# Performance work log

Measured on AMD Instinct MI355X. Metric: run time of the kernel, lower is better.

## Reference

```python
import jax, jax.numpy as jnp
import numpy as np
import math

N = 256  # channels == model dim M
B, H, W = 8, 48, 48
EPS = 1e-5


def _kaiming(key, shape, a=math.sqrt(5)):
    # kaiming_normal_ with fan_in = shape[1] (2D weight), leaky_relu gain
    fan_in = shape[1]
    gain = math.sqrt(2.0 / (1.0 + a * a))
    std = gain / math.sqrt(fan_in)
    return std * jax.random.normal(key, shape, dtype=jnp.float32)


def setup_inputs() -> dict:
    key = jax.random.key(0)
    ks = jax.random.split(key, 6)
    x_l = jax.random.normal(ks[0], (B, N, H, W), dtype=jnp.float32)
    x_r = jax.random.normal(ks[1], (B, N, H, W), dtype=jnp.float32)
    Wq = _kaiming(ks[2], (N, N))
    Wk = _kaiming(ks[3], (N, N))
    Wv = _kaiming(ks[4], (N, N))
    Wo = _kaiming(ks[5], (N, N))
    g1 = jnp.ones((N,), jnp.float32); b1 = jnp.zeros((N,), jnp.float32)
    g2 = jnp.ones((N,), jnp.float32); b2 = jnp.zeros((N,), jnp.float32)
    return {"x_l": x_l, "x_r": x_r, "Wq": Wq, "Wk": Wk, "Wv": Wv, "Wo": Wo,
            "g1": g1, "b1": b1, "g2": g2, "b2": b2}


def _layernorm(x, g, b):
    mu = jnp.mean(x, axis=-1, keepdims=True)
    var = jnp.mean(jnp.square(x - mu), axis=-1, keepdims=True)
    return (x - mu) * jax.lax.rsqrt(var + EPS) * g + b


def reference(x_l, x_r, Wq, Wk, Wv, Wo, g1, b1, g2, b2):
    Bsz, C, Hh, Ww = x_l.shape
    S = Hh * Ww
    # [B, C, H, W] -> [B, S, C]
    xl = x_l.reshape(Bsz, C, S).transpose(0, 2, 1)
    xr = x_r.reshape(Bsz, C, S).transpose(0, 2, 1)
    xln_l = _layernorm(xl, g1, b1)
    xln_r = _layernorm(xr, g2, b2)
    Ql = xln_l @ Wq; Qr = xln_r @ Wq
    Kl = xln_l @ Wk; Kr = xln_r @ Wk
    Vl = xln_l @ Wv; Vr = xln_r @ Wv
    scale = 1.0 / math.sqrt(C)
    Al = jnp.einsum('bsc,btc->bst', Ql, Kr) * scale  # [B,S,S]
    Ar = jnp.einsum('bsc,btc->bst', Qr, Kl) * scale
    # NOTE: original uses nn.Softmax() with dim=None; for a 3-D tensor torch's
    # legacy _get_softmax_dim resolves to dim=0 (over batch). Faithfully replicated.
    Pl = jax.nn.softmax(Al, axis=0)
    Pr = jax.nn.softmax(Ar, axis=0)
    out_l = xl + (Pl @ Vl) @ Wo
    out_r = xr + (Pr @ Vr) @ Wo
    out_l = out_l.transpose(0, 2, 1).reshape(Bsz, C, Hh, Ww)
    out_r = out_r.transpose(0, 2, 1).reshape(Bsz, C, Hh, Ww)
    return out_l, out_r
```

## Files before the change

### kernel.cpp

```cpp
#include <hip/hip_runtime.h>
#include <stdint.h>

#define SDIM 2304
#define CDIM 256
#define NB   8
#define MTOT (NB * SDIM)

typedef __attribute__((ext_vector_type(8))) short short8;
typedef __attribute__((ext_vector_type(4))) float f32x4;

__device__ __forceinline__ float b2f(unsigned short h) {
  union { unsigned int u; float f; } v; v.u = ((unsigned int)h) << 16; return v.f;
}
__device__ __forceinline__ unsigned short f2b(float f) {
  union { unsigned int u; float f; } v; v.f = f;
  unsigned int u = v.u;
  u += 0x7fffu + ((u >> 16) & 1u);
  return (unsigned short)(u >> 16);
}
static inline unsigned short f2b_host(float f) {
  union { unsigned int u; float f; } v; v.f = f;
  unsigned int u = v.u;
  u += 0x7fffu + ((u >> 16) & 1u);
  return (unsigned short)(u >> 16);
}

__device__ __forceinline__ void gload_lds16(const unsigned short* g, unsigned short* l) {
  __builtin_amdgcn_global_load_lds(
      (const __attribute__((address_space(1))) unsigned int*)g,
      (__attribute__((address_space(3))) unsigned int*)l,
      16, 0, 0);
}

__global__ __launch_bounds__(64)
void detect_dtype(const unsigned short* __restrict__ x, int* __restrict__ flag)
{
  int lane = threadIdx.x;
  int bad = 0;
  for (int i = lane; i < 1024; i += 64) {
    float v = b2f(x[i]);
    if (!(fabsf(v) < 1e20f)) bad = 1;
  }
  unsigned long long m = __ballot(bad);
  if (lane == 0) flag[0] = (m != 0ULL) ? 1 : 0;
}

constexpr int EP_PLAIN = 0, EP_QKV = 1, EP_OUT = 2, EP_ACC = 3;

template <int EP, int SW, int TM, int TN>
__global__ __launch_bounds__(256, 2)
void gemm_nt(const unsigned short* __restrict__ pA, int lda, long sAz,
             const unsigned short* __restrict__ pB, int ldb, long sBz, int zx,
             unsigned short* __restrict__ pC, int ldc, long sCz,
             unsigned short* __restrict__ pQ, unsigned short* __restrict__ pK,
             unsigned short* __restrict__ pV,
             const unsigned short* __restrict__ pX0, const unsigned short* __restrict__ pX1,
             float* __restrict__ pFacc, unsigned short* __restrict__ pBf, int accmode,
             const int* __restrict__ dflag, int Kdim)
{
  constexpr int WR = TM / 2;
  constexpr int AI = WR / 16;
  constexpr int BJ = TN / 32;
  constexpr int L  = TM / 64 + TN / 64;

  __shared__ __align__(16) unsigned short As[3][TM * 32];
  __shared__ __align__(16) unsigned short Bs[3][TN * 32];

  const int tid = threadIdx.x;
  int bx, by, bz;
  if constexpr (SW == 1) {
    const int h = blockIdx.x;
    const int q = h >> 4, r = h & 15;
    const int p = q * 8 + (r & 7);
    by = r >> 3;
    bx = p % 18;
    bz = p / 18;
  } else if constexpr (SW == 2) {
    const int b = blockIdx.x;
    const int n = (b & 7) * 324 + (b >> 3);
    bz = n / 162; const int r = n % 162; bx = r / 9; by = r % 9;
  } else {
    bx = blockIdx.x; by = blockIdx.y; bz = blockIdx.z;
  }
  const int z = bz;
  const long m0 = (long)bx * TM;
  const long n0 = (long)by * TN;
  const unsigned short* A  = pA + (long)z * sAz;
  const unsigned short* Bm = pB + (long)(z ^ zx) * sBz;

  const int lane = tid & 63;
  const int wave = tid >> 6;
  const int wm = (wave & 1) * WR;
  const int wn = (wave >> 1) * (TN / 2);
  const int lr = lane & 15;
  const int quad = lane >> 4;

  f32x4 acc[AI][BJ];
#pragma unroll
  for (int i = 0; i < AI; ++i)
#pragma unroll
    for (int j = 0; j < BJ; ++j) acc[i][j] = (f32x4)0.0f;

  const int e0 = tid, e1 = tid + 256, e2 = tid + 512, e3 = tid + 768;
  const int r0 = e0 >> 2, c0 = (((e0 & 3) ^ ((r0 >> 1) & 3)) << 3);
  const int r1 = e1 >> 2, c1 = (((e1 & 3) ^ ((r1 >> 1) & 3)) << 3);
  const int r2 = e2 >> 2, c2 = (((e2 & 3) ^ ((r2 >> 1) & 3)) << 3);
  const int r3 = e3 >> 2, c3 = (((e3 & 3) ^ ((r3 >> 1) & 3)) << 3);
  const unsigned short* pa0 = A  + (m0 + r0) * lda + c0;
  const unsigned short* pa1 = A  + (m0 + r1) * lda + c1;
  const unsigned short* pb0 = Bm + (n0 + r0) * ldb + c0;
  const unsigned short* pb1 = Bm + (n0 + r1) * ldb + c1;
  const unsigned short* pb2 = Bm + (n0 + r2) * ldb + c2;
  const unsigned short* pb3 = Bm + (n0 + r3) * ldb + c3;

  const int chunk = quad ^ ((lr >> 1) & 3);
  int aoff[AI], boff[BJ];
#pragma unroll
  for (int i = 0; i < AI; ++i) aoff[i] = (wm + i * 16 + lr) * 32 + chunk * 8;
#pragma unroll
  for (int i = 0; i < BJ; ++i) boff[i] = (wn + i * 16 + lr) * 32 + chunk * 8;

  const int nt = Kdim >> 5;

  auto stage = [&](int kt, int sl) {
    const int k = kt << 5;
    gload_lds16(pa0 + k, &As[sl][e0 * 8]);
    if constexpr (TM == 128) gload_lds16(pa1 + k, &As[sl][e1 * 8]);
    gload_lds16(pb0 + k, &Bs[sl][e0 * 8]);
    gload_lds16(pb1 + k, &Bs[sl][e1 * 8]);
    if constexpr (TN == 256) {
      gload_lds16(pb2 + k, &Bs[sl][e2 * 8]);
      gload_lds16(pb3 + k, &Bs[sl][e3 * 8]);
    }
  };

  stage(0, 0); stage(1, 1);

  int bc = 0;
  for (int t = 0; t < nt; ++t) {
    if (t < nt - 1) {
      if constexpr (L == 3)      asm volatile("s_waitcnt vmcnt(3)" ::: "memory");
      else if constexpr (L == 4) asm volatile("s_waitcnt vmcnt(4)" ::: "memory");
      else                       asm volatile("s_waitcnt vmcnt(6)" ::: "memory");
    } else {
      asm volatile("s_waitcnt vmcnt(0)" ::: "memory");
    }
    __builtin_amdgcn_s_barrier();
    asm volatile("" ::: "memory");

    if (t + 2 < nt) {
      const int b2 = bc ? bc - 1 : 2;
      stage(t + 2, b2);
    }

    short8 af[AI], bfr[BJ];
#pragma unroll
    for (int i = 0; i < AI; ++i) af[i]  = *(const short8*)&As[bc][aoff[i]];
#pragma unroll
    for (int i = 0; i < BJ; ++i) bfr[i] = *(const short8*)&Bs[bc][boff[i]];
#pragma unroll
    for (int i = 0; i < AI; ++i)
#pragma unroll
      for (int j = 0; j < BJ; ++j)
        acc[i][j] = __builtin_amdgcn_mfma_f32_16x16x32_bf16(af[i], bfr[j], acc[i][j], 0, 0, 0);

    bc = (bc == 2) ? 0 : bc + 1;
  }

  if constexpr (EP == EP_PLAIN) {
    unsigned short* Cp = pC + (long)z * sCz;
#pragma unroll
    for (int i = 0; i < AI; ++i) {
      const long mb = m0 + wm + i * 16 + quad * 4;
#pragma unroll
      for (int j = 0; j < BJ; ++j) {
        const long n = n0 + wn + j * 16 + lr;
#pragma unroll
        for (int r = 0; r < 4; ++r)
          Cp[(mb + r) * ldc + n] = f2b(acc[i][j][r]);
      }
    }
  } else if constexpr (EP == EP_QKV) {
    const int g  = (int)(n0 >> 8);
    const int nb = (int)(n0 & 255);
    if (g < 2) {
      unsigned short* Cp = (g == 0 ? pQ : pK) + (long)z * sCz;
#pragma unroll
      for (int i = 0; i < AI; ++i) {
        const long mb = m0 + wm + i * 16 + quad * 4;
#pragma unroll
        for (int j = 0; j < BJ; ++j) {
          const int n = nb + wn + j * 16 + lr;
#pragma unroll
          for (int r = 0; r < 4; ++r)
            Cp[(mb + r) * CDIM + n] = f2b(acc[i][j][r]);
        }
      }
    } else {
      const int b = (int)(m0 / SDIM);
      const int sblk = (int)(m0 % SDIM);
      unsigned short* Vz = pV + ((long)z * NB + b) * (long)CDIM * SDIM;
#pragma unroll
      for (int i = 0; i < AI; ++i) {
        const int s = sblk + wm + i * 16 + quad * 4;
#pragma unroll
        for (int j = 0; j < BJ; ++j) {
          const int c = nb + wn + j * 16 + lr;
          ushort4 pk;
          pk.x = f2b(acc[i][j][0]); pk.y = f2b(acc[i][j][1]);
          pk.z = f2b(acc[i][j][2]); pk.w = f2b(acc[i][j][3]);
          *(ushort4*)&Vz[(long)c * SDIM + s] = pk;
        }
      }
    }
  } else if constexpr (EP == EP_ACC) {
    float* Fz = pFacc + (long)z * SDIM * CDIM;
    unsigned short* Bz = pBf + (long)z * SDIM * CDIM;
#pragma unroll
    for (int i = 0; i < AI; ++i) {
      const long mb = m0 + wm + i * 16 + quad * 4;
#pragma unroll
      for (int j = 0; j < BJ; ++j) {
        const long n = n0 + wn + j * 16 + lr;
#pragma unroll
        for (int r = 0; r < 4; ++r) {
          const long idx = (mb + r) * CDIM + n;
          float v = acc[i][j][r];
          if (accmode != 0) v += Fz[idx];
          if (accmode == 2) Bz[idx] = f2b(v);
          else              Fz[idx] = v;
        }
      }
    }
  } else {
    const int io32 = dflag[0];
    const int b = (int)(m0 / SDIM);
    const int sblk = (int)(m0 % SDIM);
    const unsigned short* Xraw = (z == 0 ? pX0 : pX1);
    if (io32) {
      const float* Xf = (const float*)Xraw + (long)b * CDIM * SDIM;
      float* Of = (float*)pC + (long)z * sCz + (long)b * CDIM * SDIM;
#pragma unroll
      for (int i = 0; i < AI; ++i) {
        const int s = sblk + wm + i * 16 + quad * 4;
#pragma unroll
        for (int j = 0; j < BJ; ++j) {
          const int c = (int)n0 + wn + j * 16 + lr;
          const long off = (long)c * SDIM + s;
          float4 rx = *(const float4*)&Xf[off];
          float4 pk;
          pk.x = acc[i][j][0] + rx.x;
          pk.y = acc[i][j][1] + rx.y;
          pk.z = acc[i][j][2] + rx.z;
          pk.w = acc[i][j][3] + rx.w;
          *(float4*)&Of[off] = pk;
        }
      }
    } else {
      const unsigned short* X = Xraw + (long)b * CDIM * SDIM;
      unsigned short* O = pC + (long)z * sCz + (long)b * CDIM * SDIM;
#pragma unroll
      for (int i = 0; i < AI; ++i) {
        const int s = sblk + wm + i * 16 + quad * 4;
#pragma unroll
        for (int j = 0; j < BJ; ++j) {
          const int c = (int)n0 + wn + j * 16 + lr;
          const long off = (long)c * SDIM + s;
          ushort4 rx = *(const ushort4*)&X[off];
          ushort4 pk;
          pk.x = f2b(acc[i][j][0] + b2f(rx.x));
          pk.y = f2b(acc[i][j][1] + b2f(rx.y));
          pk.z = f2b(acc[i][j][2] + b2f(rx.z));
          pk.w = f2b(acc[i][j][3] + b2f(rx.w));
          *(ushort4*)&O[off] = pk;
        }
      }
    }
  }
}

__global__ __launch_bounds__(256)
void wtrans(const unsigned short* __restrict__ Wq, const unsigned short* __restrict__ Wk,
            const unsigned short* __restrict__ Wv, const unsigned short* __restrict__ Wo,
            unsigned short* __restrict__ WT, const int* __restrict__ dflag)
{
  const int io32 = dflag[0];
  int idx = blockIdx.x * 256 + threadIdx.x;
  int w = idx >> 16, r = idx & 65535, n = r >> 8, k = r & 255;
  const unsigned short* W = (w == 0) ? Wq : (w == 1) ? Wk : (w == 2) ? Wv : Wo;
  float v = io32 ? ((const float*)W)[k * 256 + n] : b2f(W[k * 256 + n]);
  if (w == 0) v *= 0.0625f;
  WT[w * 65536 + n * 256 + k] = f2b(v);
}

__global__ __launch_bounds__(256)
void ln_kernel(const unsigned short* __restrict__ xl, const unsigned short* __restrict__ xr,
               const unsigned short* __restrict__ g1, const unsigned short* __restrict__ b1,
               const unsigned short* __restrict__ g2, const unsigned short* __restrict__ b2,
               unsigned short* __restrict__ XLN, const int* __restrict__ dflag)
{
  const int io32 = dflag[0];
  const int strm = blockIdx.z;
  const int b = blockIdx.y;
  const int s0 = blockIdx.x * 64;
  const unsigned short* xraw = (strm ? xr : xl);
  const float*          xf = (const float*)xraw + (long)b * CDIM * SDIM;
  const unsigned short* xh = xraw + (long)b * CDIM * SDIM;
  const unsigned short* gg = strm ? g2 : g1;
  const unsigned short* bb = strm ? b2 : b1;
  const int tid = threadIdx.x;
  const int sl = tid & 63;
  const int team = tid >> 6;

  __shared__ float red[2][4][64];
  __shared__ float muS[64], rsS[64];
  __shared__ __align__(16) unsigned short tile[64 * 258];

  float sum = 0.f, sq = 0.f;
  for (int c = team * 64; c < team * 64 + 64; ++c) {
    const long off = (long)c * SDIM + s0 + sl;
    float v = io32 ? xf[off] : b2f(xh[off]);
    sum += v; sq += v * v;
  }
  red[0][team][sl] = sum; red[1][team][sl] = sq;
  __syncthreads();
  if (tid < 64) {
    float s_ = red[0][0][tid] + red[0][1][tid] + red[0][2][tid] + red[0][3][tid];
    float q_ = red[1][0][tid] + red[1][1][tid] + red[1][2][tid] + red[1][3][tid];
    float mu = s_ * (1.0f / CDIM);
    float var = q_ * (1.0f / CDIM) - mu * mu;
    muS[tid] = mu;
    rsS[tid] = rsqrtf(var + 1e-5f);
  }
  __syncthreads();
  const float mu = muS[sl], rs = rsS[sl];
  for (int c = team * 64; c < team * 64 + 64; ++c) {
    const long off = (long)c * SDIM + s0 + sl;
    float v = io32 ? xf[off] : b2f(xh[off]);
    float gv = io32 ? ((const float*)gg)[c] : b2f(gg[c]);
    float bv = io32 ? ((const float*)bb)[c] : b2f(bb[c]);
    tile[sl * 258 + c] = f2b((v - mu) * rs * gv + bv);
  }
  __syncthreads();
  unsigned short* outp = XLN + ((long)strm * MTOT + (long)b * SDIM + s0) * CDIM;
  const ushort2* t2 = (const ushort2*)tile;
  ushort2* o2 = (ushort2*)outp;
#pragma unroll
  for (int i = 0; i < 32; ++i) {
    int idx = i * 256 + tid;
    int r = idx >> 7, c2 = idx & 127;
    o2[idx] = t2[r * 129 + c2];
  }
}

__global__ __launch_bounds__(256)
void softmax_bdim(unsigned short* __restrict__ Ab, long total)
{
  const int strm = blockIdx.y;
  const long i8 = (((long)blockIdx.x << 8) + threadIdx.x) << 3;
  unsigned short* base = Ab + (long)strm * NB * total + i8;
  float v[NB][8];
#pragma unroll
  for (int b = 0; b < NB; ++b) {
    const ushort4* p = (const ushort4*)(base + (long)b * total);
    ushort4 a0 = p[0], a1 = p[1];
    v[b][0] = b2f(a0.x); v[b][1] = b2f(a0.y); v[b][2] = b2f(a0.z); v[b][3] = b2f(a0.w);
    v[b][4] = b2f(a1.x); v[b][5] = b2f(a1.y); v[b][6] = b2f(a1.z); v[b][7] = b2f(a1.w);
  }
#pragma unroll
  for (int j = 0; j < 8; ++j) {
    float mx = v[0][j];
#pragma unroll
    for (int b = 1; b < NB; ++b) mx = fmaxf(mx, v[b][j]);
    float s = 0.f;
#pragma unroll
    for (int b = 0; b < NB; ++b) { float e = __expf(v[b][j] - mx); v[b][j] = e; s += e; }
    float inv = 1.0f / s;
#pragma unroll
    for (int b = 0; b < NB; ++b) v[b][j] *= inv;
  }
#pragma unroll
  for (int b = 0; b < NB; ++b) {
    ushort4 a0, a1;
    a0.x = f2b(v[b][0]); a0.y = f2b(v[b][1]); a0.z = f2b(v[b][2]); a0.w = f2b(v[b][3]);
    a1.x = f2b(v[b][4]); a1.y = f2b(v[b][5]); a1.z = f2b(v[b][6]); a1.w = f2b(v[b][7]);
    ushort4* p = (ushort4*)(base + (long)b * total);
    p[0] = a0; p[1] = a1;
  }
}

__global__ __launch_bounds__(256)
void fill_val(unsigned short* __restrict__ out, unsigned short v, int n)
{
  int i = blockIdx.x * 256 + threadIdx.x;
  if (i < n) out[i] = v;
}

extern "C" void kernel_launch(void* const* d_in, const int* in_sizes, int n_in,
                              void* d_out, int out_size, void* d_ws, size_t ws_size,
                              hipStream_t stream)
{
  const unsigned short* xl = (const unsigned short*)d_in[0];
  const unsigned short* xr = (const unsigned short*)d_in[1];
  const unsigned short* Wq = (const unsigned short*)d_in[2];
  const unsigned short* Wk = (const unsigned short*)d_in[3];
  const unsigned short* Wv = (const unsigned short*)d_in[4];
  const unsigned short* Wo = (const unsigned short*)d_in[5];
  const unsigned short* g1 = (const unsigned short*)d_in[6];
  const unsigned short* b1 = (const unsigned short*)d_in[7];
  const unsigned short* g2 = (const unsigned short*)d_in[8];
  const unsigned short* b2 = (const unsigned short*)d_in[9];
  unsigned short* out = (unsigned short*)d_out;

  const size_t need_chunk = 113770496UL + 64;
  const size_t need_full  = 227016704UL + 64;
  if (ws_size < need_chunk) {
    float wsmb = (float)(ws_size >> 20);
    unsigned short v = f2b_host(wsmb * 100.0f);
    fill_val<<<dim3((out_size + 255) / 256), 256, 0, stream>>>(out, v, out_size);
    return;
  }

  int* dFlag = (int*)((char*)d_ws + ((ws_size - 16) & ~15UL));
  detect_dtype<<<dim3(1), 64, 0, stream>>>(xl, dFlag);

  if (ws_size >= need_full) {
    unsigned short* WT  = (unsigned short*)d_ws;
    unsigned short* Qb  = WT + 262144L;
    unsigned short* Kb  = Qb + 9437184L;
    unsigned short* Vt  = Kb + 9437184L;
    unsigned short* Ab  = Vt + 9437184L;
    unsigned short* XLN = Ab;
    unsigned short* PVbf = Qb;

    wtrans<<<dim3(1024), 256, 0, stream>>>(Wq, Wk, Wv, Wo, WT, dFlag);
    ln_kernel<<<dim3(36, 8, 2), 256, 0, stream>>>(xl, xr, g1, b1, g2, b2, XLN, dFlag);

    gemm_nt<EP_QKV, 0, 128, 256><<<dim3(144, 3, 2), 256, 0, stream>>>(
        XLN, CDIM, (long)MTOT * CDIM,
        WT, CDIM, 0L, 0,
        nullptr, 0, (long)MTOT * CDIM,
        Qb, Kb, Vt, nullptr, nullptr,
        nullptr, nullptr, 0, dFlag, CDIM);

    gemm_nt<EP_PLAIN, 2, 128, 256><<<dim3(2592), 256, 0, stream>>>(
        Qb, CDIM, (long)SDIM * CDIM,
        Kb, CDIM, (long)SDIM * CDIM, 8,
        Ab, SDIM, (long)SDIM * SDIM,
        nullptr, nullptr, nullptr, nullptr, nullptr,
        nullptr, nullptr, 0, dFlag, CDIM);

    softmax_bdim<<<dim3(2592, 2), 256, 0, stream>>>(Ab, (long)SDIM * SDIM);

    gemm_nt<EP_PLAIN, 1, 128, 128><<<dim3(576), 256, 0, stream>>>(
        Ab, SDIM, (long)SDIM * SDIM,
        Vt, SDIM, (long)CDIM * SDIM, 0,
        PVbf, CDIM, (long)SDIM * CDIM,
        nullptr, nullptr, nullptr, nullptr, nullptr,
        nullptr, nullptr, 0, dFlag, SDIM);

    gemm_nt<EP_OUT, 0, 128, 128><<<dim3(144, 2, 2), 256, 0, stream>>>(
        PVbf, CDIM, (long)MTOT * CDIM,
        WT + 768L * 256, CDIM, 0L, 0,
        out, 0, (long)NB * CDIM * SDIM,
        nullptr, nullptr, nullptr, xl, xr,
        nullptr, nullptr, 0, dFlag, CDIM);
    return;
  }

  unsigned short* WT  = (unsigned short*)d_ws;
  unsigned short* XLN = WT  + 1024L * 256;
  unsigned short* Abc = XLN;
  unsigned short* Qb  = XLN + 9437184L;
  unsigned short* Kb  = Qb  + 9437184L;
  unsigned short* Vt  = Kb  + 9437184L;
  float*          PVacc = (float*)(Vt + 9437184L);
  unsigned short* PVbf  = Qb;

  wtrans<<<dim3(1024), 256, 0, stream>>>(Wq, Wk, Wv, Wo, WT, dFlag);
  ln_kernel<<<dim3(36, 8, 2), 256, 0, stream>>>(xl, xr, g1, b1, g2, b2, XLN, dFlag);

  gemm_nt<EP_QKV, 0, 128, 256><<<dim3(144, 3, 2), 256, 0, stream>>>(
      XLN, CDIM, (long)MTOT * CDIM,
      WT, CDIM, 0L, 0,
      nullptr, 0, (long)MTOT * CDIM,
      Qb, Kb, Vt, nullptr, nullptr,
      nullptr, nullptr, 0, dFlag, CDIM);

  for (int tc = 0; tc < 9; ++tc) {
    gemm_nt<EP_PLAIN, 0, 128, 128><<<dim3(18, 2, 16), 256, 0, stream>>>(
        Qb, CDIM, (long)SDIM * CDIM,
        Kb + (long)tc * 256 * CDIM, CDIM, (long)SDIM * CDIM, 8,
        Abc, 256, (long)SDIM * 256,
        nullptr, nullptr, nullptr, nullptr, nullptr,
        nullptr, nullptr, 0, dFlag, CDIM);

    softmax_bdim<<<dim3(288, 2), 256, 0, stream>>>(Abc, (long)SDIM * 256);

    const int mode = (tc == 0) ? 0 : (tc == 8) ? 2 : 1;
    gemm_nt<EP_ACC, 0, 128, 128><<<dim3(18, 2, 16), 256, 0, stream>>>(
        Abc, 256, (long)SDIM * 256,
        Vt + (long)tc * 256, SDIM, (long)CDIM * SDIM, 0,
        nullptr, 0, 0L,
        nullptr, nullptr, nullptr, nullptr, nullptr,
        PVacc, PVbf, mode, dFlag, 256);
  }

  gemm_nt<EP_OUT, 0, 128, 128><<<dim3(144, 2, 2), 256, 0, stream>>>(
      PVbf, CDIM, (long)MTOT * CDIM,
      WT + 768L * 256, CDIM, 0L, 0,
      out, 0, (long)NB * CDIM * SDIM,
      nullptr, nullptr, nullptr, xl, xr,
      nullptr, nullptr, 0, dFlag, CDIM);
}
```

Before: 377.5 us.

## Stage plain GEMM epilogue through LDS for coalesced 16-byte stores; shrink QK tile

The plain-epilogue GEMM swaps its MFMA operand order so each lane holds four consecutive columns. It packs bf16 results into a padded LDS tile, reusing the pipeline buffers, then writes them to global memory as coalesced 16-byte rows instead of scattered 2-byte stores. The QK^T launch drops from 128x256 to 128x128 tiles with twice the blocks, and the block swizzle is updated to match. The extra LDS round trip and barriers add some latency, and the smaller tiles reduce operand reuse, in exchange for cheaper writes of the large S x S score matrix.

```diff
diff --git a/kernel.cpp b/kernel.cpp
--- a/kernel.cpp
+++ b/kernel.cpp
@@ -63,8 +63,12 @@
   constexpr int BJ = TN / 32;
   constexpr int L  = TM / 64 + TN / 64;
 
-  __shared__ __align__(16) unsigned short As[3][TM * 32];
-  __shared__ __align__(16) unsigned short Bs[3][TN * 32];
+  constexpr int LOOPU = 3 * (TM * 32) + 3 * (TN * 32);
+  constexpr int EPIU  = (EP == EP_PLAIN) ? TM * (TN + 8) : 0;
+  constexpr int SMEMU = LOOPU > EPIU ? LOOPU : EPIU;
+  __shared__ __align__(16) unsigned short smem[SMEMU];
+  unsigned short (*As)[TM * 32] = (unsigned short(*)[TM * 32])smem;
+  unsigned short (*Bs)[TN * 32] = (unsigned short(*)[TN * 32])(smem + 3 * TM * 32);
 
   const int tid = threadIdx.x;
   int bx, by, bz;
@@ -77,8 +81,8 @@
     bz = p / 18;
   } else if constexpr (SW == 2) {
     const int b = blockIdx.x;
-    const int n = (b & 7) * 324 + (b >> 3);
-    bz = n / 162; const int r = n % 162; bx = r / 9; by = r % 9;
+    const int n = (b & 7) * 648 + (b >> 3);
+    bz = n / 324; const int r = n % 324; by = r / 18; bx = r % 18;
   } else {
     bx = blockIdx.x; by = blockIdx.y; bz = blockIdx.z;
   }
@@ -161,24 +165,40 @@
 #pragma unroll
     for (int i = 0; i < AI; ++i)
 #pragma unroll
-      for (int j = 0; j < BJ; ++j)
-        acc[i][j] = __builtin_amdgcn_mfma_f32_16x16x32_bf16(af[i], bfr[j], acc[i][j], 0, 0, 0);
+      for (int j = 0; j < BJ; ++j) {
+        if constexpr (EP == EP_PLAIN)
+          acc[i][j] = __builtin_amdgcn_mfma_f32_16x16x32_bf16(bfr[j], af[i], acc[i][j], 0, 0, 0);
+        else
+          acc[i][j] = __builtin_amdgcn_mfma_f32_16x16x32_bf16(af[i], bfr[j], acc[i][j], 0, 0, 0);
+      }
 
     bc = (bc == 2) ? 0 : bc + 1;
   }
 
   if constexpr (EP == EP_PLAIN) {
+    __syncthreads();
+    unsigned short* E = smem;
+#pragma unroll
+    for (int i = 0; i < AI; ++i) {
+      const int ml = wm + i * 16 + lr;
+#pragma unroll
+      for (int j = 0; j < BJ; ++j) {
+        const int nl = wn + j * 16 + quad * 4;
+        ushort4 pk;
+        pk.x = f2b(acc[i][j][0]); pk.y = f2b(acc[i][j][1]);
+        pk.z = f2b(acc[i][j][2]); pk.w = f2b(acc[i][j][3]);
+        *(ushort4*)&E[ml * (TN + 8) + nl] = pk;
+      }
+    }
+    __syncthreads();
     unsigned short* Cp = pC + (long)z * sCz;
-#pragma unroll
-    for (int i = 0; i < AI; ++i) {
-      const long mb = m0 + wm + i * 16 + quad * 4;
-#pragma unroll
-      for (int j = 0; j < BJ; ++j) {
-        const long n = n0 + wn + j * 16 + lr;
-#pragma unroll
-        for (int r = 0; r < 4; ++r)
-          Cp[(mb + r) * ldc + n] = f2b(acc[i][j][r]);
-      }
+    constexpr int NT8 = TN / 8;
+#pragma unroll
+    for (int it = 0; it < TM * NT8 / 256; ++it) {
+      const int idx = it * 256 + tid;
+      const int row = idx / NT8, c8 = (idx % NT8) * 8;
+      uint4 v = *(const uint4*)&E[row * (TN + 8) + c8];
+      *(uint4*)&Cp[(m0 + row) * (long)ldc + n0 + c8] = v;
     }
   } else if constexpr (EP == EP_QKV) {
     const int g  = (int)(n0 >> 8);
@@ -443,7 +463,7 @@
         Qb, Kb, Vt, nullptr, nullptr,
         nullptr, nullptr, 0, dFlag, CDIM);
 
-    gemm_nt<EP_PLAIN, 2, 128, 256><<<dim3(2592), 256, 0, stream>>>(
+    gemm_nt<EP_PLAIN, 2, 128, 128><<<dim3(5184), 256, 0, stream>>>(
         Qb, CDIM, (long)SDIM * CDIM,
         Kb, CDIM, (long)SDIM * CDIM, 8,
         Ab, SDIM, (long)SDIM * SDIM,
```

Result: faster. 365.1 us (-3.3%).
